# Optimization experiments

Measured on AMD Instinct MI355X. Metric: run time of the kernel, lower is better.

The kernel has to match this reference:

```python
import jax, jax.numpy as jnp
import numpy as np

N = 100000
E = 300000
IN_C = 256
HID = 256   # 2 * out_channels
OUT_C = 128


def setup_inputs() -> dict:
    key = jax.random.key(0)
    k1, k2, k3, k4, k5 = jax.random.split(key, 5)
    x = jax.random.normal(k1, (N, IN_C), dtype=jnp.float32)
    edge_index = jax.random.randint(k2, (2, E), 0, N, dtype=jnp.int64)
    # Glorot-style init scale for GEMM weights
    W1 = jax.random.normal(k3, (IN_C, HID), dtype=jnp.float32) * (1.0 / np.sqrt(IN_C))
    b1 = jnp.zeros((HID,), dtype=jnp.float32)
    W2 = jax.random.normal(k4, (HID, OUT_C), dtype=jnp.float32) * (1.0 / np.sqrt(HID))
    b2 = jnp.zeros((OUT_C,), dtype=jnp.float32)
    return {"x": x, "edge_index": edge_index, "W1": W1, "b1": b1, "W2": W2, "b2": b2}


def _gcn_conv(x, W, b, src, dst, norm, n_nodes):
    # x: [N, Fin] -> transform then gather-scale-scatter aggregate
    h = x @ W                                   # [N, Fout]
    msgs = h[src] * norm[:, None]               # [E+N, Fout] (includes self-loops)
    out = jax.ops.segment_sum(msgs, dst, num_segments=n_nodes)
    return out + b


def _gcn_norm(edge_index, n_nodes):
    # add self-loops, compute symmetric deg^-1/2 normalization (PyG GCNConv default)
    loops = jnp.arange(n_nodes, dtype=edge_index.dtype)
    src = jnp.concatenate([edge_index[0], loops])
    dst = jnp.concatenate([edge_index[1], loops])
    deg = jax.ops.segment_sum(jnp.ones_like(dst, dtype=jnp.float32), dst, num_segments=n_nodes)
    dinv = jnp.where(deg > 0, jax.lax.rsqrt(deg), 0.0)
    norm = dinv[src] * dinv[dst]                # [E+N]
    return src, dst, norm


def reference(x, edge_index, W1, b1, W2, b2):
    n_nodes = x.shape[0]
    src, dst, norm = _gcn_norm(edge_index, n_nodes)
    h = _gcn_conv(x, W1, b1, src, dst, norm, n_nodes)
    h = jax.nn.relu(h)
    # dropout is identity in eval mode (reference baseline runs deterministic eval)
    return _gcn_conv(h, W2, b2, src, dst, norm, n_nodes)
```

## Files before the change

### kernel.cpp

```cpp
#include <hip/hip_runtime.h>
#include <stdint.h>

#define IN_C  256
#define HID   256
#define OUT_C 128
#define SCAN_BS 1024

typedef __bf16 bf16x8 __attribute__((ext_vector_type(8)));
typedef float  f32x4  __attribute__((ext_vector_type(4)));
typedef unsigned short u16x8 __attribute__((ext_vector_type(8)));
typedef unsigned short u16x4 __attribute__((ext_vector_type(4)));
typedef unsigned short u16x2 __attribute__((ext_vector_type(2)));
typedef unsigned int u32;

static __device__ __forceinline__ unsigned short f2b(float f) {
    union { float f; uint32_t u; } v; v.f = f;
    uint32_t r = v.u + 0x7fffu + ((v.u >> 16) & 1u);
    return (unsigned short)(r >> 16);
}
static __device__ __forceinline__ float b2f(unsigned short b) {
    union { uint32_t u; float f; } v; v.u = ((uint32_t)b) << 16;
    return v.f;
}
static __device__ __forceinline__ u32 cvtpk(float lo, float hi) {
    u32 r;
    asm("v_cvt_pk_bf16_f32 %0, %1, %2" : "=v"(r) : "v"(lo), "v"(hi));
    return r;
}

typedef __attribute__((address_space(1))) const u32 gas_u32;
typedef __attribute__((address_space(3))) u32 las_u32;
static __device__ __forceinline__ void gld16(const void* g, void* l) {
    __builtin_amdgcn_global_load_lds((gas_u32*)g, (las_u32*)l, 16, 0, 0);
}

__global__ void k_init(const float* __restrict__ W1, const float* __restrict__ W2,
                       unsigned short* __restrict__ W1G, unsigned short* __restrict__ W2T,
                       int* __restrict__ cnt, int n) {
    int i = blockIdx.x * blockDim.x + threadIdx.x;
    if (i < 65536) {
        int gi = i >> 3, j = i & 7;
        int kt = gi >> 10, c = (gi >> 8) & 3, nn = gi & 255;
        int k = kt * 32 + c * 8 + j;
        W1G[i] = f2b(W1[(size_t)k * HID + nn]);
    }
    if (i < 32768) W2T[i] = f2b(W2[(i & 255) * OUT_C + (i >> 8)]);
    if (i < n) cnt[i] = 0;
}

__global__ void k_count(const int* __restrict__ dst, int* __restrict__ cnt, int e) {
    int i = blockIdx.x * blockDim.x + threadIdx.x;
    if (i < e) atomicAdd(&cnt[dst[i]], 1);
}

__global__ __launch_bounds__(SCAN_BS) void k_scan_block(
    const int* __restrict__ cnt, int* __restrict__ rs, int* __restrict__ bsum, int n) {
    __shared__ int s[SCAN_BS];
    const int tid = threadIdx.x;
    const int i = blockIdx.x * SCAN_BS + tid;
    int v = (i < n) ? cnt[i] + 1 : 0;
    s[tid] = v;
    __syncthreads();
    for (int off = 1; off < SCAN_BS; off <<= 1) {
        int t = (tid >= off) ? s[tid - off] : 0;
        __syncthreads();
        s[tid] += t;
        __syncthreads();
    }
    if (i < n) rs[i] = s[tid] - v;
    if (tid == SCAN_BS - 1) bsum[blockIdx.x] = s[tid];
}

__global__ void k_scan_sums(int* __restrict__ bsum, int nb) {
    __shared__ int s[128];
    const int tid = threadIdx.x;
    int v = (tid < nb) ? bsum[tid] : 0;
    s[tid] = v;
    __syncthreads();
    for (int off = 1; off < 128; off <<= 1) {
        int t = (tid >= off) ? s[tid - off] : 0;
        __syncthreads();
        s[tid] += t;
        __syncthreads();
    }
    if (tid < nb) bsum[tid] = s[tid] - v;
}

__global__ void k_scan_add(int* __restrict__ rs, int* __restrict__ cur,
                           const int* __restrict__ bsum, const int* __restrict__ cnt,
                           float* __restrict__ dinv, int2* __restrict__ csrw, int n) {
    int i = blockIdx.x * blockDim.x + threadIdx.x;
    if (i < n) {
        int v = rs[i] + bsum[i >> 10];
        rs[i] = v;
        cur[i] = v + 1;
        float dp1 = (float)(cnt[i] + 1);
        dinv[i] = rsqrtf(dp1);
        csrw[v] = make_int2(i, __float_as_int(1.0f / dp1));
    }
}

__global__ void k_fill(const int* __restrict__ src, const int* __restrict__ dst,
                       const float* __restrict__ dinv,
                       int* __restrict__ cur, int2* __restrict__ csrw, int e) {
    int i = blockIdx.x * blockDim.x + threadIdx.x;
    if (i < e) {
        int s = src[i], d = dst[i];
        int p = atomicAdd(&cur[d], 1);
        csrw[p] = make_int2(s, __float_as_int(dinv[s] * dinv[d]));
    }
}

__global__ __launch_bounds__(512) void k_gemm1(
    const float* __restrict__ x, const unsigned short* __restrict__ W1G,
    unsigned short* __restrict__ t1, int n) {
    __shared__ __align__(16) unsigned short As[2][4096];
    __shared__ __align__(16) unsigned short Bs[2][8192];
    const int tid  = threadIdx.x;
    const int row0 = blockIdx.x * 128;
    const int wid = tid >> 6, lane = tid & 63;
    const int wm = wid >> 2, wn = wid & 3;
    const int lrow = lane & 15, lgrp = lane >> 4;

    const int ar = tid & 127, ac = tid >> 7;
    int arow = row0 + ar; if (arow > n - 1) arow = n - 1;
    const float* aptr = x + (size_t)arow * IN_C + ac * 8;

    f32x4 acc[4][4];
    #pragma unroll
    for (int i = 0; i < 4; ++i)
        #pragma unroll
        for (int j = 0; j < 4; ++j)
            acc[i][j] = (f32x4){0.f, 0.f, 0.f, 0.f};

    {
        #pragma unroll
        for (int i = 0; i < 2; ++i) {
            int chunk = tid + 512 * i;
            gld16(&W1G[(size_t)chunk * 8], &Bs[0][chunk * 8]);
        }
        f32x4 a = *(const f32x4*)aptr;
        f32x4 b = *(const f32x4*)(aptr + 4);
        union { u32 w[4]; u16x8 v; } pk;
        pk.w[0] = cvtpk(a[0], a[1]); pk.w[1] = cvtpk(a[2], a[3]);
        pk.w[2] = cvtpk(b[0], b[1]); pk.w[3] = cvtpk(b[2], b[3]);
        *(u16x8*)&As[0][ac * 1024 + ar * 8] = pk.v;
    }
    __syncthreads();

    int cur = 0;
    for (int kt = 0; kt < 8; ++kt) {
        const int nxt = cur ^ 1;
        f32x4 pa, pb;
        const bool more = (kt < 7);
        if (more) {
            #pragma unroll
            for (int i = 0; i < 2; ++i) {
                int chunk = tid + 512 * i;
                gld16(&W1G[(size_t)(kt + 1) * 8192 + chunk * 8], &Bs[nxt][chunk * 8]);
            }
            const float* ap = aptr + (kt + 1) * 32;
            pa = *(const f32x4*)ap;
            pb = *(const f32x4*)(ap + 4);
        }
        bf16x8 av[4], bv[4];
        #pragma unroll
        for (int mf = 0; mf < 4; ++mf) {
            int r = wm * 64 + mf * 16 + lrow;
            av[mf] = *(const bf16x8*)&As[cur][lgrp * 1024 + r * 8];
        }
        #pragma unroll
        for (int nf = 0; nf < 4; ++nf) {
            int cc = wn * 64 + nf * 16 + lrow;
            bv[nf] = *(const bf16x8*)&Bs[cur][lgrp * 2048 + cc * 8];
        }
        #pragma unroll
        for (int mf = 0; mf < 4; ++mf)
            #pragma unroll
            for (int nf = 0; nf < 4; ++nf)
                acc[mf][nf] = __builtin_amdgcn_mfma_f32_16x16x32_bf16(
                    av[mf], bv[nf], acc[mf][nf], 0, 0, 0);
        if (more) {
            union { u32 w[4]; u16x8 v; } pk;
            pk.w[0] = cvtpk(pa[0], pa[1]); pk.w[1] = cvtpk(pa[2], pa[3]);
            pk.w[2] = cvtpk(pb[0], pb[1]); pk.w[3] = cvtpk(pb[2], pb[3]);
            *(u16x8*)&As[nxt][ac * 1024 + ar * 8] = pk.v;
        }
        __syncthreads();
        cur = nxt;
    }

    #pragma unroll
    for (int mf = 0; mf < 4; ++mf)
        #pragma unroll
        for (int j = 0; j < 4; ++j) {
            int grow = row0 + wm * 64 + mf * 16 + lgrp * 4 + j;
            if (grow < n) {
                #pragma unroll
                for (int nf = 0; nf < 4; ++nf) {
                    int col = wn * 64 + nf * 16 + lrow;
                    t1[(size_t)grow * HID + col] = f2b(acc[mf][nf][j]);
                }
            }
        }
}

__global__ __launch_bounds__(256) void k_agg1(
    const unsigned short* __restrict__ t1, const int* __restrict__ rs,
    const int* __restrict__ cnt, const int2* __restrict__ csrw,
    const float* __restrict__ b1, unsigned short* __restrict__ out1, int n) {
    const int w = blockIdx.x * 4 + (threadIdx.x >> 6);
    const int n0 = w * 4;
    if (n0 >= n) return;
    const int lane = threadIdx.x & 63;
    const int ch = lane * 4;
    int beg[4], m[4];
    #pragma unroll
    for (int q = 0; q < 4; ++q) {
        int node = n0 + q;
        bool valid = node < n;
        beg[q] = valid ? rs[node] : 0;
        m[q]   = valid ? cnt[node] + 1 : 0;
    }
    float acc[4][4];
    #pragma unroll
    for (int q = 0; q < 4; ++q)
        #pragma unroll
        for (int k = 0; k < 4; ++k) acc[q][k] = 0.f;
    const int m01 = m[0] > m[1] ? m[0] : m[1];
    const int m23 = m[2] > m[3] ? m[2] : m[3];
    const int mmax = m01 > m23 ? m01 : m23;
    for (int j = 0; j < mmax; ++j) {
        #pragma unroll
        for (int q = 0; q < 4; ++q) {
            if (j < m[q]) {
                int2 p = csrw[beg[q] + j];
                float wq = __int_as_float(p.y);
                u16x4 u = *(const u16x4*)&t1[(size_t)p.x * HID + ch];
                acc[q][0] += b2f(u[0]) * wq; acc[q][1] += b2f(u[1]) * wq;
                acc[q][2] += b2f(u[2]) * wq; acc[q][3] += b2f(u[3]) * wq;
            }
        }
    }
    float4 bb = *(const float4*)(b1 + ch);
    #pragma unroll
    for (int q = 0; q < 4; ++q) {
        int node = n0 + q;
        if (node < n) {
            u16x4 o;
            o[0] = f2b(fmaxf(acc[q][0] + bb.x, 0.f));
            o[1] = f2b(fmaxf(acc[q][1] + bb.y, 0.f));
            o[2] = f2b(fmaxf(acc[q][2] + bb.z, 0.f));
            o[3] = f2b(fmaxf(acc[q][3] + bb.w, 0.f));
            *(u16x4*)&out1[(size_t)node * HID + ch] = o;
        }
    }
}

__global__ __launch_bounds__(256) void k_gemm2(
    const unsigned short* __restrict__ out1, const unsigned short* __restrict__ W2T,
    unsigned short* __restrict__ t2, int n) {
    __shared__ __align__(16) unsigned short As[128 * 64];
    __shared__ __align__(16) unsigned short Bs[128 * 64];
    const int tid  = threadIdx.x;
    const int row0 = blockIdx.x * 128;
    const int wid = tid >> 6, lane = tid & 63;
    const int wm = wid >> 1, wn = wid & 1;
    const int lrow = lane & 15, lgrp = lane >> 4;

    f32x4 acc[4][4];
    #pragma unroll
    for (int i = 0; i < 4; ++i)
        #pragma unroll
        for (int j = 0; j < 4; ++j)
            acc[i][j] = (f32x4){0.f, 0.f, 0.f, 0.f};

    for (int kt = 0; kt < 4; ++kt) {
        #pragma unroll
        for (int i = 0; i < 4; ++i) {
            int chunk = tid + 256 * i;
            int r = chunk >> 3, c = chunk & 7;
            int grow = row0 + r; if (grow > n - 1) grow = n - 1;
            gld16(&out1[(size_t)grow * HID + kt * 64 + ((c ^ (r & 7)) * 8)],
                  &As[chunk * 8]);
        }
        #pragma unroll
        for (int i = 0; i < 4; ++i) {
            int chunk = tid + 256 * i;
            int nn = chunk >> 3, c = chunk & 7;
            gld16(&W2T[(size_t)nn * 256 + kt * 64 + ((c ^ (nn & 7)) * 8)],
                  &Bs[chunk * 8]);
        }
        __syncthreads();
        #pragma unroll
        for (int kk = 0; kk < 2; ++kk) {
            const int cfrag = kk * 4 + lgrp;
            bf16x8 av[4], bv[4];
            #pragma unroll
            for (int mf = 0; mf < 4; ++mf) {
                int r = wm * 64 + mf * 16 + lrow;
                av[mf] = *(const bf16x8*)&As[r * 64 + ((cfrag ^ (r & 7)) * 8)];
            }
            #pragma unroll
            for (int nf = 0; nf < 4; ++nf) {
                int cc = wn * 64 + nf * 16 + lrow;
                bv[nf] = *(const bf16x8*)&Bs[cc * 64 + ((cfrag ^ (cc & 7)) * 8)];
            }
            #pragma unroll
            for (int mf = 0; mf < 4; ++mf)
                #pragma unroll
                for (int nf = 0; nf < 4; ++nf)
                    acc[mf][nf] = __builtin_amdgcn_mfma_f32_16x16x32_bf16(
                        av[mf], bv[nf], acc[mf][nf], 0, 0, 0);
        }
        __syncthreads();
    }
    #pragma unroll
    for (int mf = 0; mf < 4; ++mf)
        #pragma unroll
        for (int j = 0; j < 4; ++j) {
            int grow = row0 + wm * 64 + mf * 16 + lgrp * 4 + j;
            if (grow < n) {
                #pragma unroll
                for (int nf = 0; nf < 4; ++nf) {
                    int col = wn * 64 + nf * 16 + lrow;
                    t2[(size_t)grow * OUT_C + col] = f2b(acc[mf][nf][j]);
                }
            }
        }
}

__global__ __launch_bounds__(256) void k_agg2(
    const unsigned short* __restrict__ t2, const int* __restrict__ rs,
    const int* __restrict__ cnt, const int2* __restrict__ csrw,
    const float* __restrict__ b2, float* __restrict__ out, int n) {
    const int w = blockIdx.x * 4 + (threadIdx.x >> 6);
    const int n0 = w * 4;
    if (n0 >= n) return;
    const int lane = threadIdx.x & 63;
    const int ch = lane * 2;
    int beg[4], m[4];
    #pragma unroll
    for (int q = 0; q < 4; ++q) {
        int node = n0 + q;
        bool valid = node < n;
        beg[q] = valid ? rs[node] : 0;
        m[q]   = valid ? cnt[node] + 1 : 0;
    }
    float acc[4][2];
    #pragma unroll
    for (int q = 0; q < 4; ++q) { acc[q][0] = 0.f; acc[q][1] = 0.f; }
    const int m01 = m[0] > m[1] ? m[0] : m[1];
    const int m23 = m[2] > m[3] ? m[2] : m[3];
    const int mmax = m01 > m23 ? m01 : m23;
    for (int j = 0; j < mmax; ++j) {
        #pragma unroll
        for (int q = 0; q < 4; ++q) {
            if (j < m[q]) {
                int2 p = csrw[beg[q] + j];
                float wq = __int_as_float(p.y);
                u16x2 u = *(const u16x2*)&t2[(size_t)p.x * OUT_C + ch];
                acc[q][0] += b2f(u[0]) * wq; acc[q][1] += b2f(u[1]) * wq;
            }
        }
    }
    float2 bb = *(const float2*)(b2 + ch);
    #pragma unroll
    for (int q = 0; q < 4; ++q) {
        int node = n0 + q;
        if (node < n)
            *(float2*)&out[(size_t)node * OUT_C + ch] =
                make_float2(acc[q][0] + bb.x, acc[q][1] + bb.y);
    }
}

extern "C" void kernel_launch(void* const* d_in, const int* in_sizes, int n_in,
                              void* d_out, int out_size, void* d_ws, size_t ws_size,
                              hipStream_t stream) {
    const float* x  = (const float*)d_in[0];
    const int*   ei = (const int*)d_in[1];
    const float* W1 = (const float*)d_in[2];
    const float* b1 = (const float*)d_in[3];
    const float* W2 = (const float*)d_in[4];
    const float* b2 = (const float*)d_in[5];
    float* out = (float*)d_out;

    const int n = in_sizes[0] / IN_C;
    const int e = in_sizes[1] / 2;
    const int* src = ei;
    const int* dst = ei + e;

    int*   cnt  = (int*)d_ws;
    int*   rs   = cnt + n;
    int*   cur  = rs + n;
    int*   bsum = cur + n;
    float* dinv = (float*)(bsum + 128);
    int2*  csrw = (int2*)(dinv + n);
    unsigned short* W1G = (unsigned short*)(csrw + (size_t)e + n);
    unsigned short* W2T = W1G + 65536;
    unsigned short* t1  = W2T + 32768;
    unsigned short* out1 = t1 + (size_t)n * HID;
    unsigned short* t2  = t1;

    const int nb = (n + SCAN_BS - 1) / SCAN_BS;

    k_init<<<(n + 255) / 256, 256, 0, stream>>>(W1, W2, W1G, W2T, cnt, n);
    k_count<<<(e + 255) / 256, 256, 0, stream>>>(dst, cnt, e);
    k_scan_block<<<nb, SCAN_BS, 0, stream>>>(cnt, rs, bsum, n);
    k_scan_sums<<<1, 128, 0, stream>>>(bsum, nb);
    k_scan_add<<<(n + 255) / 256, 256, 0, stream>>>(rs, cur, bsum, cnt, dinv, csrw, n);
    k_fill<<<(e + 255) / 256, 256, 0, stream>>>(src, dst, dinv, cur, csrw, e);

    const int mb = (n + 127) / 128;
    k_gemm1<<<mb, 512, 0, stream>>>(x, W1G, t1, n);
    const int aggblk = (n + 15) / 16;
    k_agg1<<<aggblk, 256, 0, stream>>>(t1, rs, cnt, csrw, b1, out1, n);
    k_gemm2<<<mb, 256, 0, stream>>>(out1, W2T, t2, n);
    k_agg2<<<aggblk, 256, 0, stream>>>(t2, rs, cnt, csrw, b2, out, n);
}
```

Measured before the change: 209.4 us.

## Fuse CSR build preprocessing into a single cooperative kernel with grid syncs

Replaces six small launches with one cooperative kernel: weight conversion, zeroing of counts, degree counting, a two-level scan, dinv computation and the CSR fill. Phases are separated by grid.sync(). The aim is to remove per-launch overhead and the gaps between launches in the graph-building stage. The trade-offs are grid-wide barrier costs and a fixed grid of 1024 blocks, which caps n at 262144 for the single-pass scan.

```diff
diff --git a/kernel.cpp b/kernel.cpp
--- a/kernel.cpp
+++ b/kernel.cpp
@@ -1,10 +1,13 @@
 #include <hip/hip_runtime.h>
+#include <hip/hip_cooperative_groups.h>
 #include <stdint.h>
+
+namespace cg = cooperative_groups;
 
 #define IN_C  256
 #define HID   256
 #define OUT_C 128
-#define SCAN_BS 1024
+#define NBLD  1024
 
 typedef __bf16 bf16x8 __attribute__((ext_vector_type(8)));
 typedef float  f32x4  __attribute__((ext_vector_type(4)));
@@ -34,80 +37,81 @@
     __builtin_amdgcn_global_load_lds((gas_u32*)g, (las_u32*)l, 16, 0, 0);
 }
 
-__global__ void k_init(const float* __restrict__ W1, const float* __restrict__ W2,
-                       unsigned short* __restrict__ W1G, unsigned short* __restrict__ W2T,
-                       int* __restrict__ cnt, int n) {
-    int i = blockIdx.x * blockDim.x + threadIdx.x;
-    if (i < 65536) {
+__global__ __launch_bounds__(256) void k_build(
+    const int* __restrict__ src, const int* __restrict__ dst,
+    const float* __restrict__ W1, const float* __restrict__ W2,
+    int* __restrict__ cnt, int* __restrict__ rs, int* __restrict__ cur,
+    int* __restrict__ bsum, float* __restrict__ dinv, int2* __restrict__ csrw,
+    unsigned short* __restrict__ W1G, unsigned short* __restrict__ W2T,
+    int n, int e) {
+    cg::grid_group grid = cg::this_grid();
+    const int tid = threadIdx.x;
+    const int gid = blockIdx.x * 256 + tid;
+    const int gsz = NBLD * 256;
+
+    for (int i = gid; i < 65536; i += gsz) {
         int gi = i >> 3, j = i & 7;
         int kt = gi >> 10, c = (gi >> 8) & 3, nn = gi & 255;
-        int k = kt * 32 + c * 8 + j;
-        W1G[i] = f2b(W1[(size_t)k * HID + nn]);
-    }
-    if (i < 32768) W2T[i] = f2b(W2[(i & 255) * OUT_C + (i >> 8)]);
-    if (i < n) cnt[i] = 0;
-}
-
-__global__ void k_count(const int* __restrict__ dst, int* __restrict__ cnt, int e) {
-    int i = blockIdx.x * blockDim.x + threadIdx.x;
-    if (i < e) atomicAdd(&cnt[dst[i]], 1);
-}
-
-__global__ __launch_bounds__(SCAN_BS) void k_scan_block(
-    const int* __restrict__ cnt, int* __restrict__ rs, int* __restrict__ bsum, int n) {
-    __shared__ int s[SCAN_BS];
-    const int tid = threadIdx.x;
-    const int i = blockIdx.x * SCAN_BS + tid;
-    int v = (i < n) ? cnt[i] + 1 : 0;
+        W1G[i] = f2b(W1[(size_t)(kt * 32 + c * 8 + j) * HID + nn]);
+    }
+    for (int i = gid; i < 32768; i += gsz)
+        W2T[i] = f2b(W2[(i & 255) * OUT_C + (i >> 8)]);
+    for (int i = gid; i < n; i += gsz) cnt[i] = 0;
+    grid.sync();
+
+    for (int i = gid; i < e; i += gsz) atomicAdd(&cnt[dst[i]], 1);
+    grid.sync();
+
+    __shared__ int s[256];
+    int v = (gid < n) ? cnt[gid] + 1 : 0;
     s[tid] = v;
     __syncthreads();
-    for (int off = 1; off < SCAN_BS; off <<= 1) {
+    #pragma unroll
+    for (int off = 1; off < 256; off <<= 1) {
         int t = (tid >= off) ? s[tid - off] : 0;
         __syncthreads();
         s[tid] += t;
         __syncthreads();
     }
-    if (i < n) rs[i] = s[tid] - v;
-    if (tid == SCAN_BS - 1) bsum[blockIdx.x] = s[tid];
-}
-
-__global__ void k_scan_sums(int* __restrict__ bsum, int nb) {
-    __shared__ int s[128];
-    const int tid = threadIdx.x;
-    int v = (tid < nb) ? bsum[tid] : 0;
-    s[tid] = v;
-    __syncthreads();
-    for (int off = 1; off < 128; off <<= 1) {
-        int t = (tid >= off) ? s[tid - off] : 0;
-        __syncthreads();
-        s[tid] += t;
-        __syncthreads();
-    }
-    if (tid < nb) bsum[tid] = s[tid] - v;
-}
-
-__global__ void k_scan_add(int* __restrict__ rs, int* __restrict__ cur,
-                           const int* __restrict__ bsum, const int* __restrict__ cnt,
-                           float* __restrict__ dinv, int2* __restrict__ csrw, int n) {
-    int i = blockIdx.x * blockDim.x + threadIdx.x;
-    if (i < n) {
-        int v = rs[i] + bsum[i >> 10];
-        rs[i] = v;
-        cur[i] = v + 1;
-        float dp1 = (float)(cnt[i] + 1);
-        dinv[i] = rsqrtf(dp1);
-        csrw[v] = make_int2(i, __float_as_int(1.0f / dp1));
-    }
-}
-
-__global__ void k_fill(const int* __restrict__ src, const int* __restrict__ dst,
-                       const float* __restrict__ dinv,
-                       int* __restrict__ cur, int2* __restrict__ csrw, int e) {
-    int i = blockIdx.x * blockDim.x + threadIdx.x;
-    if (i < e) {
-        int s = src[i], d = dst[i];
+    const int lexcl = s[tid] - v;
+    if (tid == 255) bsum[blockIdx.x] = s[255];
+    grid.sync();
+
+    if (blockIdx.x == 0) {
+        int l0 = bsum[tid * 4], l1 = bsum[tid * 4 + 1];
+        int l2 = bsum[tid * 4 + 2], l3 = bsum[tid * 4 + 3];
+        int tot = l0 + l1 + l2 + l3;
+        s[tid] = tot;
+        __syncthreads();
+        #pragma unroll
+        for (int off = 1; off < 256; off <<= 1) {
+            int t = (tid >= off) ? s[tid - off] : 0;
+            __syncthreads();
+            s[tid] += t;
+            __syncthreads();
+        }
+        int base = s[tid] - tot;
+        bsum[tid * 4]     = base;
+        bsum[tid * 4 + 1] = base + l0;
+        bsum[tid * 4 + 2] = base + l0 + l1;
+        bsum[tid * 4 + 3] = base + l0 + l1 + l2;
+    }
+    grid.sync();
+
+    if (gid < n) {
+        int p = lexcl + bsum[blockIdx.x];
+        rs[gid] = p;
+        cur[gid] = p + 1;
+        float dp1 = (float)(cnt[gid] + 1);
+        dinv[gid] = rsqrtf(dp1);
+        csrw[p] = make_int2(gid, __float_as_int(1.0f / dp1));
+    }
+    grid.sync();
+
+    for (int i = gid; i < e; i += gsz) {
+        int sN = src[i], d = dst[i];
         int p = atomicAdd(&cur[d], 1);
-        csrw[p] = make_int2(s, __float_as_int(dinv[s] * dinv[d]));
+        csrw[p] = make_int2(sN, __float_as_int(dinv[sN] * dinv[d]));
     }
 }
 
@@ -385,8 +389,8 @@
     const float* b2 = (const float*)d_in[5];
     float* out = (float*)d_out;
 
-    const int n = in_sizes[0] / IN_C;
-    const int e = in_sizes[1] / 2;
+    int n = in_sizes[0] / IN_C;
+    int e = in_sizes[1] / 2;
     const int* src = ei;
     const int* dst = ei + e;
 
@@ -394,7 +398,7 @@
     int*   rs   = cnt + n;
     int*   cur  = rs + n;
     int*   bsum = cur + n;
-    float* dinv = (float*)(bsum + 128);
+    float* dinv = (float*)(bsum + NBLD);
     int2*  csrw = (int2*)(dinv + n);
     unsigned short* W1G = (unsigned short*)(csrw + (size_t)e + n);
     unsigned short* W2T = W1G + 65536;
@@ -402,14 +406,14 @@
     unsigned short* out1 = t1 + (size_t)n * HID;
     unsigned short* t2  = t1;
 
-    const int nb = (n + SCAN_BS - 1) / SCAN_BS;
-
-    k_init<<<(n + 255) / 256, 256, 0, stream>>>(W1, W2, W1G, W2T, cnt, n);
-    k_count<<<(e + 255) / 256, 256, 0, stream>>>(dst, cnt, e);
-    k_scan_block<<<nb, SCAN_BS, 0, stream>>>(cnt, rs, bsum, n);
-    k_scan_sums<<<1, 128, 0, stream>>>(bsum, nb);
-    k_scan_add<<<(n + 255) / 256, 256, 0, stream>>>(rs, cur, bsum, cnt, dinv, csrw, n);
-    k_fill<<<(e + 255) / 256, 256, 0, stream>>>(src, dst, dinv, cur, csrw, e);
+    void* args[] = {
+        (void*)&src, (void*)&dst, (void*)&W1, (void*)&W2,
+        (void*)&cnt, (void*)&rs, (void*)&cur, (void*)&bsum,
+        (void*)&dinv, (void*)&csrw, (void*)&W1G, (void*)&W2T,
+        (void*)&n, (void*)&e
+    };
+    hipLaunchCooperativeKernel((void*)k_build, dim3(NBLD), dim3(256),
+                               args, 0, stream);
 
     const int mb = (n + 127) / 128;
     k_gemm1<<<mb, 512, 0, stream>>>(x, W1G, t1, n);
```

New measurement: 689.4 us. 3.29x slower.

## Replace three-kernel prefix scan with atomic segment allocation for CSR rows

Applied to the files above, without the earlier changes.

Drops the block scan, block-sum scan and add kernels that built CSR row offsets. In their place, one kernel reserves each node's segment with an atomicAdd on a global counter, so CSR rows are still contiguous but no longer in node order. This removes two kernel launches and the scan's barrier-heavy work. The cost is heavy contention on a single atomic across all nodes, and a nondeterministic row layout that can hurt locality in the aggregation kernels.

```diff
diff --git a/kernel.cpp b/kernel.cpp
--- a/kernel.cpp
+++ b/kernel.cpp
@@ -4,7 +4,6 @@
 #define IN_C  256
 #define HID   256
 #define OUT_C 128
-#define SCAN_BS 1024
 
 typedef __bf16 bf16x8 __attribute__((ext_vector_type(8)));
 typedef float  f32x4  __attribute__((ext_vector_type(4)));
@@ -36,16 +35,16 @@
 
 __global__ void k_init(const float* __restrict__ W1, const float* __restrict__ W2,
                        unsigned short* __restrict__ W1G, unsigned short* __restrict__ W2T,
-                       int* __restrict__ cnt, int n) {
+                       int* __restrict__ cnt, int* __restrict__ total, int n) {
     int i = blockIdx.x * blockDim.x + threadIdx.x;
     if (i < 65536) {
         int gi = i >> 3, j = i & 7;
         int kt = gi >> 10, c = (gi >> 8) & 3, nn = gi & 255;
-        int k = kt * 32 + c * 8 + j;
-        W1G[i] = f2b(W1[(size_t)k * HID + nn]);
+        W1G[i] = f2b(W1[(size_t)(kt * 32 + c * 8 + j) * HID + nn]);
     }
     if (i < 32768) W2T[i] = f2b(W2[(i & 255) * OUT_C + (i >> 8)]);
     if (i < n) cnt[i] = 0;
+    if (i == 0) *total = 0;
 }
 
 __global__ void k_count(const int* __restrict__ dst, int* __restrict__ cnt, int e) {
@@ -53,50 +52,18 @@
     if (i < e) atomicAdd(&cnt[dst[i]], 1);
 }
 
-__global__ __launch_bounds__(SCAN_BS) void k_scan_block(
-    const int* __restrict__ cnt, int* __restrict__ rs, int* __restrict__ bsum, int n) {
-    __shared__ int s[SCAN_BS];
-    const int tid = threadIdx.x;
-    const int i = blockIdx.x * SCAN_BS + tid;
-    int v = (i < n) ? cnt[i] + 1 : 0;
-    s[tid] = v;
-    __syncthreads();
-    for (int off = 1; off < SCAN_BS; off <<= 1) {
-        int t = (tid >= off) ? s[tid - off] : 0;
-        __syncthreads();
-        s[tid] += t;
-        __syncthreads();
-    }
-    if (i < n) rs[i] = s[tid] - v;
-    if (tid == SCAN_BS - 1) bsum[blockIdx.x] = s[tid];
-}
-
-__global__ void k_scan_sums(int* __restrict__ bsum, int nb) {
-    __shared__ int s[128];
-    const int tid = threadIdx.x;
-    int v = (tid < nb) ? bsum[tid] : 0;
-    s[tid] = v;
-    __syncthreads();
-    for (int off = 1; off < 128; off <<= 1) {
-        int t = (tid >= off) ? s[tid - off] : 0;
-        __syncthreads();
-        s[tid] += t;
-        __syncthreads();
-    }
-    if (tid < nb) bsum[tid] = s[tid] - v;
-}
-
-__global__ void k_scan_add(int* __restrict__ rs, int* __restrict__ cur,
-                           const int* __restrict__ bsum, const int* __restrict__ cnt,
-                           float* __restrict__ dinv, int2* __restrict__ csrw, int n) {
+__global__ void k_alloc(int* __restrict__ rs, int* __restrict__ cur,
+                        const int* __restrict__ cnt, int* __restrict__ total,
+                        float* __restrict__ dinv, int2* __restrict__ csrw, int n) {
     int i = blockIdx.x * blockDim.x + threadIdx.x;
     if (i < n) {
-        int v = rs[i] + bsum[i >> 10];
-        rs[i] = v;
-        cur[i] = v + 1;
-        float dp1 = (float)(cnt[i] + 1);
+        int m = cnt[i] + 1;
+        int p = atomicAdd(total, m);
+        rs[i] = p;
+        cur[i] = p + 1;
+        float dp1 = (float)m;
         dinv[i] = rsqrtf(dp1);
-        csrw[v] = make_int2(i, __float_as_int(1.0f / dp1));
+        csrw[p] = make_int2(i, __float_as_int(1.0f / dp1));
     }
 }
 
@@ -393,8 +360,8 @@
     int*   cnt  = (int*)d_ws;
     int*   rs   = cnt + n;
     int*   cur  = rs + n;
-    int*   bsum = cur + n;
-    float* dinv = (float*)(bsum + 128);
+    int*   total = cur + n;
+    float* dinv = (float*)(total + 4);
     int2*  csrw = (int2*)(dinv + n);
     unsigned short* W1G = (unsigned short*)(csrw + (size_t)e + n);
     unsigned short* W2T = W1G + 65536;
@@ -402,13 +369,9 @@
     unsigned short* out1 = t1 + (size_t)n * HID;
     unsigned short* t2  = t1;
 
-    const int nb = (n + SCAN_BS - 1) / SCAN_BS;
-
-    k_init<<<(n + 255) / 256, 256, 0, stream>>>(W1, W2, W1G, W2T, cnt, n);
+    k_init<<<(n + 255) / 256, 256, 0, stream>>>(W1, W2, W1G, W2T, cnt, total, n);
     k_count<<<(e + 255) / 256, 256, 0, stream>>>(dst, cnt, e);
-    k_scan_block<<<nb, SCAN_BS, 0, stream>>>(cnt, rs, bsum, n);
-    k_scan_sums<<<1, 128, 0, stream>>>(bsum, nb);
-    k_scan_add<<<(n + 255) / 256, 256, 0, stream>>>(rs, cur, bsum, cnt, dinv, csrw, n);
+    k_alloc<<<(n + 255) / 256, 256, 0, stream>>>(rs, cur, cnt, total, dinv, csrw, n);
     k_fill<<<(e + 255) / 256, 256, 0, stream>>>(src, dst, dinv, cur, csrw, e);
 
     const int mb = (n + 127) / 128;
```

New measurement: 233.0 us. 1.11x slower.
